# Optimization experiments

Measured on AMD Instinct MI355X. Metric: run time of the kernel, lower is better.

## Reference

```python
import jax, jax.numpy as jnp
import numpy as np

N_NODES = 100000
N_EDGES = 1600000
IN_F, HID_F, OUT_F = 128, 128, 64


def setup_inputs() -> dict:
    key = jax.random.key(0)
    ks = jax.random.split(key, 12)
    inp = {
        "features": jax.random.normal(ks[0], (N_NODES, IN_F), dtype=jnp.float32),
        "src": jax.random.randint(ks[1], (N_EDGES,), 0, N_NODES, dtype=jnp.int32),
        "dst": jax.random.randint(ks[2], (N_EDGES,), 0, N_NODES, dtype=jnp.int32),
        "Ws0": jax.random.normal(ks[3], (IN_F, HID_F), dtype=jnp.float32) / np.sqrt(IN_F),
        "Wn0": jax.random.normal(ks[4], (IN_F, HID_F), dtype=jnp.float32) / np.sqrt(IN_F),
        "b0": jnp.zeros((HID_F,), dtype=jnp.float32),
        "Ws1": jax.random.normal(ks[5], (HID_F, HID_F), dtype=jnp.float32) / np.sqrt(HID_F),
        "Wn1": jax.random.normal(ks[6], (HID_F, HID_F), dtype=jnp.float32) / np.sqrt(HID_F),
        "b1": jnp.zeros((HID_F,), dtype=jnp.float32),
        "Ws2": jax.random.normal(ks[7], (HID_F, OUT_F), dtype=jnp.float32) / np.sqrt(HID_F),
        "Wn2": jax.random.normal(ks[8], (HID_F, OUT_F), dtype=jnp.float32) / np.sqrt(HID_F),
        "b2": jnp.zeros((OUT_F,), dtype=jnp.float32),
    }
    return inp


def _sage_conv(h, src, dst, inv_deg, Ws, Wn, b, act):
    # gather neighbor (source) features along edges: [E, d]
    msg = h[src]
    # mean aggregation onto destination nodes: [N, d]
    agg = jax.ops.segment_sum(msg, dst, num_segments=N_NODES) * inv_deg
    out = h @ Ws + agg @ Wn + b
    return jax.nn.relu(out) if act else out


def reference(features, src, dst, Ws0, Wn0, b0, Ws1, Wn1, b1, Ws2, Wn2, b2):
    # in-degree for mean normalization (clamped at 1, matching DGL mean semantics)
    deg = jax.ops.segment_sum(jnp.ones((N_EDGES,), jnp.float32), dst, num_segments=N_NODES)
    inv_deg = (1.0 / jnp.maximum(deg, 1.0))[:, None]
    h = _sage_conv(features, src, dst, inv_deg, Ws0, Wn0, b0, act=True)
    # dropout is identity in eval mode
    h = _sage_conv(h, src, dst, inv_deg, Ws1, Wn1, b1, act=True)
    h = _sage_conv(h, src, dst, inv_deg, Ws2, Wn2, b2, act=False)
    return h
```

## Files before the change

### kernel.cpp

```cpp
#include <hip/hip_runtime.h>

static constexpr int N = 100000;
static constexpr int E = 1600000;
static constexpr int F = 128;
static constexpr int HA_W = 256;
static constexpr int NB = (N + 127) / 128;
static constexpr int PCHUNK = 16384;
static constexpr int PGRID = (E + PCHUNK - 1) / PCHUNK;
static constexpr int CAP = 8192;

typedef __attribute__((ext_vector_type(8))) short bf16x8;
typedef __attribute__((ext_vector_type(4))) float f32x4;

__device__ inline unsigned short f2bf(float f) {
    unsigned int u = __builtin_bit_cast(unsigned int, f);
    unsigned int r = u + 0x7FFF + ((u >> 16) & 1);
    return (unsigned short)(r >> 16);
}
__device__ inline float bf_lo(unsigned int v) {
    return __builtin_bit_cast(float, v << 16);
}
__device__ inline float bf_hi(unsigned int v) {
    return __builtin_bit_cast(float, v & 0xffff0000u);
}

__global__ __launch_bounds__(256) void bucket_count_k(const int* __restrict__ dst,
                                                      int* __restrict__ bcnt) {
    __shared__ int sh[NB];
    const int t = threadIdx.x;
    for (int i = t; i < NB; i += 256) sh[i] = 0;
    __syncthreads();
    const int cb = blockIdx.x * PCHUNK;
    #pragma unroll
    for (int j = 0; j < PCHUNK / 1024; ++j) {
        int idx = cb + j * 1024 + t * 4;
        if (idx < E) {
            int4 d4 = *(const int4*)&dst[idx];
            atomicAdd(&sh[d4.x >> 7], 1);
            atomicAdd(&sh[d4.y >> 7], 1);
            atomicAdd(&sh[d4.z >> 7], 1);
            atomicAdd(&sh[d4.w >> 7], 1);
        }
    }
    __syncthreads();
    for (int i = t; i < NB; i += 256)
        if (sh[i]) atomicAdd(&bcnt[i], sh[i]);
}

__global__ __launch_bounds__(1024) void scan_buckets_k(const int* __restrict__ bcnt,
                                                       int* __restrict__ bbase,
                                                       int* __restrict__ bcur,
                                                       int* __restrict__ row_ptr) {
    __shared__ int shw[16];
    const int t = threadIdx.x, lane = t & 63, wv = t >> 6;
    int v = (t < NB) ? bcnt[t] : 0;
    int s = v;
    #pragma unroll
    for (int off = 1; off < 64; off <<= 1) {
        int u = __shfl_up(s, off);
        if (lane >= off) s += u;
    }
    if (lane == 63) shw[wv] = s;
    __syncthreads();
    if (wv == 0 && lane < 16) {
        int w = shw[lane];
        #pragma unroll
        for (int off = 1; off < 16; off <<= 1) {
            int u = __shfl_up(w, off);
            if (lane >= off) w += u;
        }
        shw[lane] = w;
    }
    __syncthreads();
    int wex = wv ? shw[wv - 1] : 0;
    int excl = wex + s - v;
    if (t < NB) { bbase[t] = excl; bcur[t] = 0; }
    if (t == 0) { bbase[NB] = E; row_ptr[N] = E; }
}

__global__ __launch_bounds__(256) void partition_k(const int* __restrict__ src,
                                                   const int* __restrict__ dst,
                                                   const int* __restrict__ bbase,
                                                   int* __restrict__ bcur,
                                                   unsigned int* __restrict__ ebuf) {
    __shared__ int sh_hist[NB];
    __shared__ int sh_base[NB];
    __shared__ int sh_cur[NB];
    const int t = threadIdx.x;
    for (int i = t; i < NB; i += 256) sh_hist[i] = 0;
    __syncthreads();
    const int cb = blockIdx.x * PCHUNK;
    #pragma unroll
    for (int j = 0; j < PCHUNK / 1024; ++j) {
        int idx = cb + j * 1024 + t * 4;
        if (idx < E) {
            int4 d4 = *(const int4*)&dst[idx];
            atomicAdd(&sh_hist[d4.x >> 7], 1);
            atomicAdd(&sh_hist[d4.y >> 7], 1);
            atomicAdd(&sh_hist[d4.z >> 7], 1);
            atomicAdd(&sh_hist[d4.w >> 7], 1);
        }
    }
    __syncthreads();
    for (int i = t; i < NB; i += 256) {
        int c = sh_hist[i];
        sh_base[i] = c ? (bbase[i] + atomicAdd(&bcur[i], c)) : 0;
        sh_cur[i] = 0;
    }
    __syncthreads();
    #pragma unroll
    for (int j = 0; j < PCHUNK / 1024; ++j) {
        int idx = cb + j * 1024 + t * 4;
        if (idx < E) {
            int4 s4 = *(const int4*)&src[idx];
            int4 d4 = *(const int4*)&dst[idx];
            {
                int b = d4.x >> 7; int p = atomicAdd(&sh_cur[b], 1);
                ebuf[sh_base[b] + p] = (unsigned)s4.x | ((unsigned)(d4.x & 127) << 17);
            }
            {
                int b = d4.y >> 7; int p = atomicAdd(&sh_cur[b], 1);
                ebuf[sh_base[b] + p] = (unsigned)s4.y | ((unsigned)(d4.y & 127) << 17);
            }
            {
                int b = d4.z >> 7; int p = atomicAdd(&sh_cur[b], 1);
                ebuf[sh_base[b] + p] = (unsigned)s4.z | ((unsigned)(d4.z & 127) << 17);
            }
            {
                int b = d4.w >> 7; int p = atomicAdd(&sh_cur[b], 1);
                ebuf[sh_base[b] + p] = (unsigned)s4.w | ((unsigned)(d4.w & 127) << 17);
            }
        }
    }
}

__global__ __launch_bounds__(256) void csr_sort_k(const unsigned int* __restrict__ ebuf,
                                                  const int* __restrict__ bbase,
                                                  int* __restrict__ row_ptr,
                                                  float* __restrict__ inv_deg,
                                                  int* __restrict__ esrc) {
    __shared__ unsigned int sh_e[CAP];
    __shared__ int sh_o[CAP];
    __shared__ int sh_hist[128];
    __shared__ int sh_excl[128];
    __shared__ int sh_cur[128];
    __shared__ int sh_w0;
    const int b = blockIdx.x, t = threadIdx.x;
    const int e0 = bbase[b];
    const int ec = bbase[b + 1] - e0;
    if (t < 128) { sh_hist[t] = 0; sh_cur[t] = 0; }
    __syncthreads();
    for (int i = t; i < ec; i += 256) {
        unsigned int e = ebuf[e0 + i];
        sh_e[i] = e;
        atomicAdd(&sh_hist[e >> 17], 1);
    }
    __syncthreads();
    int v = 0;
    if (t < 128) v = sh_hist[t];
    int incl = v;
    const int lane = t & 63;
    #pragma unroll
    for (int off = 1; off < 64; off <<= 1) {
        int u = __shfl_up(incl, off);
        if (lane >= off) incl += u;
    }
    if (t == 63) sh_w0 = incl;
    __syncthreads();
    if (t >= 64 && t < 128) incl += sh_w0;
    if (t < 128) {
        sh_excl[t] = incl - v;
        int node = b * 128 + t;
        if (node < N) {
            row_ptr[node] = e0 + incl - v;
            inv_deg[node] = 1.0f / fmaxf((float)v, 1.0f);
        }
    }
    __syncthreads();
    for (int i = t; i < ec; i += 256) {
        unsigned int e = sh_e[i];
        int l = e >> 17;
        int pos = sh_excl[l] + atomicAdd(&sh_cur[l], 1);
        sh_o[pos] = (int)(e & 0x1FFFF);
    }
    __syncthreads();
    for (int i = t; i < ec; i += 256) esrc[e0 + i] = sh_o[i];
}

__global__ __launch_bounds__(256) void conv_feat_k(const float* __restrict__ feat,
                                                   unsigned short* __restrict__ ha) {
    int idx = blockIdx.x * 256 + threadIdx.x;
    int node = idx >> 5;
    int c4 = idx & 31;
    if (node >= N) return;
    float4 v = *(const float4*)&feat[(size_t)node * F + c4 * 4];
    unsigned long long p = (unsigned long long)f2bf(v.x)
                         | ((unsigned long long)f2bf(v.y) << 16)
                         | ((unsigned long long)f2bf(v.z) << 32)
                         | ((unsigned long long)f2bf(v.w) << 48);
    *(unsigned long long*)&ha[(size_t)node * HA_W + c4 * 4] = p;
}

__global__ __launch_bounds__(256) void prep_w_all_k(const float* __restrict__ Ws0,
                                                    const float* __restrict__ Wn0,
                                                    const float* __restrict__ Ws1,
                                                    const float* __restrict__ Wn1,
                                                    const float* __restrict__ Ws2,
                                                    const float* __restrict__ Wn2,
                                                    unsigned short* __restrict__ Wt0,
                                                    unsigned short* __restrict__ Wt1,
                                                    unsigned short* __restrict__ Wc2) {
    int idx = blockIdx.x * 256 + threadIdx.x;
    if (idx < 32768) {
        int n = idx >> 8, k = idx & 255;
        float v = (k < 128) ? Ws0[k * 128 + n] : Wn0[(k - 128) * 128 + n];
        Wt0[n * 256 + k] = f2bf(v);
    } else if (idx < 65536) {
        int j = idx - 32768;
        int n = j >> 8, k = j & 255;
        float v = (k < 128) ? Ws1[k * 128 + n] : Wn1[(k - 128) * 128 + n];
        Wt1[n * 256 + k] = f2bf(v);
    } else if (idx < 65536 + 16384) {
        int j = idx - 65536;
        int c = j >> 7, k = j & 127;
        float v = (c < 64) ? Ws2[k * 64 + c] : Wn2[k * 64 + (c - 64)];
        Wc2[c * 128 + k] = f2bf(v);
    }
}

__global__ __launch_bounds__(256) void aggregate128_k(const unsigned short* __restrict__ ha,
                                                      unsigned short* __restrict__ ha_out,
                                                      const int* __restrict__ row_ptr,
                                                      const int* __restrict__ esrc,
                                                      const float* __restrict__ inv_deg) {
    const int lane = threadIdx.x & 63;
    const int wv = threadIdx.x >> 6;
    const int slot = lane >> 4;
    const int cl = lane & 15;
    const int node = blockIdx.x * 16 + wv * 4 + slot;
    const int beg = row_ptr[node];
    const int cnt = row_ptr[node + 1] - beg;
    const float sinv = inv_deg[node];
    int wmax = cnt;
    wmax = max(wmax, __shfl_xor(wmax, 16));
    wmax = max(wmax, __shfl_xor(wmax, 32));
    float a0 = 0.f, a1 = 0.f, a2 = 0.f, a3 = 0.f;
    float a4 = 0.f, a5 = 0.f, a6 = 0.f, a7 = 0.f;
    for (int j = 0; j < wmax; j += 8) {
        int idx[8];
        uint4 v[8];
        #pragma unroll
        for (int u = 0; u < 8; ++u)
            idx[u] = (j + u < cnt) ? __builtin_nontemporal_load(&esrc[beg + j + u]) : -1;
        #pragma unroll
        for (int u = 0; u < 8; ++u) {
            if (idx[u] >= 0)
                v[u] = *(const uint4*)&ha[(size_t)idx[u] * HA_W + cl * 8];
            else { v[u].x = 0u; v[u].y = 0u; v[u].z = 0u; v[u].w = 0u; }
        }
        #pragma unroll
        for (int u = 0; u < 8; ++u) {
            a0 += bf_lo(v[u].x); a1 += bf_hi(v[u].x);
            a2 += bf_lo(v[u].y); a3 += bf_hi(v[u].y);
            a4 += bf_lo(v[u].z); a5 += bf_hi(v[u].z);
            a6 += bf_lo(v[u].w); a7 += bf_hi(v[u].w);
        }
    }
    uint4 o;
    o.x = (unsigned int)f2bf(a0 * sinv) | ((unsigned int)f2bf(a1 * sinv) << 16);
    o.y = (unsigned int)f2bf(a2 * sinv) | ((unsigned int)f2bf(a3 * sinv) << 16);
    o.z = (unsigned int)f2bf(a4 * sinv) | ((unsigned int)f2bf(a5 * sinv) << 16);
    o.w = (unsigned int)f2bf(a6 * sinv) | ((unsigned int)f2bf(a7 * sinv) << 16);
    *(uint4*)&ha_out[(size_t)node * HA_W + F + cl * 8] = o;
}

__global__ __launch_bounds__(256) void aggregate64_add_k(const unsigned short* __restrict__ Q,
                                                         const int* __restrict__ row_ptr,
                                                         const int* __restrict__ esrc,
                                                         const float* __restrict__ inv_deg,
                                                         float* __restrict__ out) {
    const int lane = threadIdx.x & 63;
    const int wv = threadIdx.x >> 6;
    const int slot = lane >> 3;
    const int cl = lane & 7;
    const int node = blockIdx.x * 32 + wv * 8 + slot;
    const int beg = row_ptr[node];
    const int cnt = row_ptr[node + 1] - beg;
    const float sinv = inv_deg[node];
    int wmax = cnt;
    wmax = max(wmax, __shfl_xor(wmax, 8));
    wmax = max(wmax, __shfl_xor(wmax, 16));
    wmax = max(wmax, __shfl_xor(wmax, 32));
    float a0 = 0.f, a1 = 0.f, a2 = 0.f, a3 = 0.f;
    float a4 = 0.f, a5 = 0.f, a6 = 0.f, a7 = 0.f;
    for (int j = 0; j < wmax; j += 8) {
        int idx[8];
        uint4 v[8];
        #pragma unroll
        for (int u = 0; u < 8; ++u)
            idx[u] = (j + u < cnt) ? __builtin_nontemporal_load(&esrc[beg + j + u]) : -1;
        #pragma unroll
        for (int u = 0; u < 8; ++u) {
            if (idx[u] >= 0)
                v[u] = *(const uint4*)&Q[(size_t)idx[u] * 64 + cl * 8];
            else { v[u].x = 0u; v[u].y = 0u; v[u].z = 0u; v[u].w = 0u; }
        }
        #pragma unroll
        for (int u = 0; u < 8; ++u) {
            a0 += bf_lo(v[u].x); a1 += bf_hi(v[u].x);
            a2 += bf_lo(v[u].y); a3 += bf_hi(v[u].y);
            a4 += bf_lo(v[u].z); a5 += bf_hi(v[u].z);
            a6 += bf_lo(v[u].w); a7 += bf_hi(v[u].w);
        }
    }
    float4* p0 = (float4*)&out[(size_t)node * 64 + cl * 8];
    float4 pv = *p0;
    pv.x += a0 * sinv; pv.y += a1 * sinv; pv.z += a2 * sinv; pv.w += a3 * sinv;
    *p0 = pv;
    float4* p1 = p0 + 1;
    float4 pw = *p1;
    pw.x += a4 * sinv; pw.y += a5 * sinv; pw.z += a6 * sinv; pw.w += a7 * sinv;
    *p1 = pw;
}

__global__ __launch_bounds__(256) void linear01_k(const unsigned short* __restrict__ ha,
                                                  const unsigned short* __restrict__ Wt,
                                                  const float* __restrict__ bias,
                                                  unsigned short* __restrict__ out_ha) {
    constexpr int CPW = 32;
    constexpr int NT = 2;
    const int lane = threadIdx.x & 63;
    const int wv = threadIdx.x >> 6;
    const int col0 = wv * CPW;
    const int lc = lane & 15;
    const int lg = lane >> 4;
    bf16x8 bfrag[NT][8];
    float bias_c[NT];
    #pragma unroll
    for (int nt = 0; nt < NT; ++nt) {
        int col = col0 + nt * 16 + lc;
        bias_c[nt] = bias[col];
        #pragma unroll
        for (int ks = 0; ks < 8; ++ks)
            bfrag[nt][ks] = *(const bf16x8*)&Wt[col * 256 + ks * 32 + lg * 8];
    }
    const int i0base = blockIdx.x * 128;
    for (int s = 0; s < 8; ++s) {
        int i0 = i0base + s * 16;
        if (i0 >= N) return;
        const unsigned short* arow = &ha[(size_t)(i0 + lc) * HA_W];
        f32x4 acc[NT];
        #pragma unroll
        for (int nt = 0; nt < NT; ++nt) {
            acc[nt][0] = bias_c[nt]; acc[nt][1] = bias_c[nt];
            acc[nt][2] = bias_c[nt]; acc[nt][3] = bias_c[nt];
        }
        #pragma unroll
        for (int ks = 0; ks < 8; ++ks) {
            bf16x8 af = *(const bf16x8*)&arow[ks * 32 + lg * 8];
            #pragma unroll
            for (int nt = 0; nt < NT; ++nt)
                acc[nt] = __builtin_amdgcn_mfma_f32_16x16x32_bf16(af, bfrag[nt][ks], acc[nt], 0, 0, 0);
        }
        #pragma unroll
        for (int nt = 0; nt < NT; ++nt) {
            int col = col0 + nt * 16 + lc;
            #pragma unroll
            for (int r = 0; r < 4; ++r) {
                int orow = i0 + lg * 4 + r;
                float v = fmaxf(acc[nt][r], 0.f);
                out_ha[(size_t)orow * HA_W + col] = f2bf(v);
            }
        }
    }
}

__global__ __launch_bounds__(256) void linear2_k(const unsigned short* __restrict__ ha,
                                                 const unsigned short* __restrict__ Wc,
                                                 const float* __restrict__ bias,
                                                 float* __restrict__ out,
                                                 unsigned short* __restrict__ Q) {
    constexpr int CPW = 32;
    constexpr int NT = 2;
    const int lane = threadIdx.x & 63;
    const int wv = threadIdx.x >> 6;
    const int col0 = wv * CPW;
    const int lc = lane & 15;
    const int lg = lane >> 4;
    bf16x8 bfrag[NT][4];
    float bias_c[NT];
    #pragma unroll
    for (int nt = 0; nt < NT; ++nt) {
        int col = col0 + nt * 16 + lc;
        bias_c[nt] = (wv < 2) ? bias[col] : 0.f;
        #pragma unroll
        for (int ks = 0; ks < 4; ++ks)
            bfrag[nt][ks] = *(const bf16x8*)&Wc[col * 128 + ks * 32 + lg * 8];
    }
    const int i0base = blockIdx.x * 128;
    for (int s = 0; s < 8; ++s) {
        int i0 = i0base + s * 16;
        if (i0 >= N) return;
        const unsigned short* arow = &ha[(size_t)(i0 + lc) * HA_W];
        f32x4 acc[NT];
        #pragma unroll
        for (int nt = 0; nt < NT; ++nt) {
            acc[nt][0] = bias_c[nt]; acc[nt][1] = bias_c[nt];
            acc[nt][2] = bias_c[nt]; acc[nt][3] = bias_c[nt];
        }
        #pragma unroll
        for (int ks = 0; ks < 4; ++ks) {
            bf16x8 af = *(const bf16x8*)&arow[ks * 32 + lg * 8];
            #pragma unroll
            for (int nt = 0; nt < NT; ++nt)
                acc[nt] = __builtin_amdgcn_mfma_f32_16x16x32_bf16(af, bfrag[nt][ks], acc[nt], 0, 0, 0);
        }
        #pragma unroll
        for (int nt = 0; nt < NT; ++nt) {
            int col = col0 + nt * 16 + lc;
            #pragma unroll
            for (int r = 0; r < 4; ++r) {
                int orow = i0 + lg * 4 + r;
                float v = acc[nt][r];
                if (wv < 2) out[(size_t)orow * 64 + col] = v;
                else        Q[(size_t)orow * 64 + (col - 64)] = f2bf(v);
            }
        }
    }
}

extern "C" void kernel_launch(void* const* d_in, const int* in_sizes, int n_in,
                              void* d_out, int out_size, void* d_ws, size_t ws_size,
                              hipStream_t stream) {
    const float* feat = (const float*)d_in[0];
    const int*   src  = (const int*)d_in[1];
    const int*   dst  = (const int*)d_in[2];
    const float* Ws0  = (const float*)d_in[3];
    const float* Wn0  = (const float*)d_in[4];
    const float* b0   = (const float*)d_in[5];
    const float* Ws1  = (const float*)d_in[6];
    const float* Wn1  = (const float*)d_in[7];
    const float* b1   = (const float*)d_in[8];
    const float* Ws2  = (const float*)d_in[9];
    const float* Wn2  = (const float*)d_in[10];
    const float* b2   = (const float*)d_in[11];
    float* out = (float*)d_out;

    char* ws = (char*)d_ws;
    size_t off = 0;
    auto alloc = [&](size_t bytes) {
        void* p = ws + off;
        off = (off + bytes + 255) & ~(size_t)255;
        return p;
    };
    unsigned short* haA = (unsigned short*)alloc((size_t)N * HA_W * 2);
    unsigned short* haB = (unsigned short*)alloc((size_t)N * HA_W * 2);
    unsigned short* Qb  = (unsigned short*)alloc((size_t)N * 64 * 2);
    unsigned short* Wt0 = (unsigned short*)alloc((size_t)128 * 256 * 2);
    unsigned short* Wt1 = (unsigned short*)alloc((size_t)128 * 256 * 2);
    unsigned short* Wc2 = (unsigned short*)alloc((size_t)128 * 128 * 2);
    float* inv     = (float*)alloc((size_t)N * 4);
    int*   row_ptr = (int*)alloc((size_t)(N + 1) * 4);
    int*   bcnt    = (int*)alloc((size_t)NB * 4);
    int*   bbase   = (int*)alloc((size_t)(NB + 1) * 4);
    int*   bcur    = (int*)alloc((size_t)NB * 4);
    unsigned int* ebuf = (unsigned int*)alloc((size_t)E * 4);
    int*   esrc    = (int*)alloc((size_t)E * 4);
    (void)ws_size; (void)in_sizes; (void)n_in; (void)out_size;

    hipMemsetAsync(bcnt, 0, (size_t)NB * 4, stream);
    bucket_count_k<<<PGRID, 256, 0, stream>>>(dst, bcnt);
    scan_buckets_k<<<1, 1024, 0, stream>>>(bcnt, bbase, bcur, row_ptr);
    partition_k<<<PGRID, 256, 0, stream>>>(src, dst, bbase, bcur, ebuf);
    csr_sort_k<<<NB, 256, 0, stream>>>(ebuf, bbase, row_ptr, inv, esrc);

    conv_feat_k<<<(N * 32 + 255) / 256, 256, 0, stream>>>(feat, haA);
    prep_w_all_k<<<(65536 + 16384 + 255) / 256, 256, 0, stream>>>(
        Ws0, Wn0, Ws1, Wn1, Ws2, Wn2, Wt0, Wt1, Wc2);

    const int lin_grid = (N + 127) / 128;
    aggregate128_k<<<N / 16, 256, 0, stream>>>(haA, haA, row_ptr, esrc, inv);
    linear01_k<<<lin_grid, 256, 0, stream>>>(haA, Wt0, b0, haB);
    aggregate128_k<<<N / 16, 256, 0, stream>>>(haB, haB, row_ptr, esrc, inv);
    linear01_k<<<lin_grid, 256, 0, stream>>>(haB, Wt1, b1, haA);
    linear2_k<<<lin_grid, 256, 0, stream>>>(haA, Wc2, b2, out, Qb);
    aggregate64_add_k<<<N / 32, 256, 0, stream>>>(Qb, row_ptr, esrc, inv, out);
}
```

Before: 326.1 us.

## Fuse aggregation with linear layer via LDS and merge prep kernels

Fuses mean-aggregation and the dense linear for layers 0 and 1 into one 512-thread kernel. Each block aggregates 128 nodes into shared memory and then runs MFMA on the self features from global memory plus the aggregated tile from LDS. The feature buffers shrink from 256 to 128 columns because the aggregate no longer round-trips through global memory. Feature conversion, bucket counting and weight prep are merged into one launch. The fused kernel has only NB (~782) blocks, which may cut gather parallelism and latency hiding compared with the old 6250-block aggregate kernel.

New measurement: 328.5 us. About the same (+0.8%).

```diff
diff --git a/kernel.cpp b/kernel.cpp
--- a/kernel.cpp
+++ b/kernel.cpp
@@ -3,11 +3,11 @@
 static constexpr int N = 100000;
 static constexpr int E = 1600000;
 static constexpr int F = 128;
-static constexpr int HA_W = 256;
 static constexpr int NB = (N + 127) / 128;
 static constexpr int PCHUNK = 16384;
 static constexpr int PGRID = (E + PCHUNK - 1) / PCHUNK;
 static constexpr int CAP = 8192;
+static constexpr int NPAD = NB * 128;
 
 typedef __attribute__((ext_vector_type(8))) short bf16x8;
 typedef __attribute__((ext_vector_type(4))) float f32x4;
@@ -24,27 +24,70 @@
     return __builtin_bit_cast(float, v & 0xffff0000u);
 }
 
-__global__ __launch_bounds__(256) void bucket_count_k(const int* __restrict__ dst,
-                                                      int* __restrict__ bcnt) {
+__global__ __launch_bounds__(256) void prep_all_k(const float* __restrict__ feat,
+                                                  unsigned short* __restrict__ hA,
+                                                  const int* __restrict__ dst,
+                                                  int* __restrict__ bcnt,
+                                                  const float* __restrict__ Ws0,
+                                                  const float* __restrict__ Wn0,
+                                                  const float* __restrict__ Ws1,
+                                                  const float* __restrict__ Wn1,
+                                                  const float* __restrict__ Ws2,
+                                                  const float* __restrict__ Wn2,
+                                                  unsigned short* __restrict__ Wt0,
+                                                  unsigned short* __restrict__ Wt1,
+                                                  unsigned short* __restrict__ Wc2) {
     __shared__ int sh[NB];
     const int t = threadIdx.x;
-    for (int i = t; i < NB; i += 256) sh[i] = 0;
-    __syncthreads();
-    const int cb = blockIdx.x * PCHUNK;
-    #pragma unroll
-    for (int j = 0; j < PCHUNK / 1024; ++j) {
-        int idx = cb + j * 1024 + t * 4;
-        if (idx < E) {
-            int4 d4 = *(const int4*)&dst[idx];
-            atomicAdd(&sh[d4.x >> 7], 1);
-            atomicAdd(&sh[d4.y >> 7], 1);
-            atomicAdd(&sh[d4.z >> 7], 1);
-            atomicAdd(&sh[d4.w >> 7], 1);
-        }
-    }
-    __syncthreads();
-    for (int i = t; i < NB; i += 256)
-        if (sh[i]) atomicAdd(&bcnt[i], sh[i]);
+    const int bid = blockIdx.x;
+    if (bid < 12500) {
+        int idx = bid * 256 + t;
+        int node = idx >> 5;
+        int c4 = idx & 31;
+        if (node < N) {
+            float4 v = *(const float4*)&feat[(size_t)node * F + c4 * 4];
+            unsigned long long p = (unsigned long long)f2bf(v.x)
+                                 | ((unsigned long long)f2bf(v.y) << 16)
+                                 | ((unsigned long long)f2bf(v.z) << 32)
+                                 | ((unsigned long long)f2bf(v.w) << 48);
+            *(unsigned long long*)&hA[(size_t)node * F + c4 * 4] = p;
+        }
+    } else if (bid < 12500 + PGRID) {
+        for (int i = t; i < NB; i += 256) sh[i] = 0;
+        __syncthreads();
+        const int cb = (bid - 12500) * PCHUNK;
+        #pragma unroll
+        for (int j = 0; j < PCHUNK / 1024; ++j) {
+            int idx = cb + j * 1024 + t * 4;
+            if (idx < E) {
+                int4 d4 = *(const int4*)&dst[idx];
+                atomicAdd(&sh[d4.x >> 7], 1);
+                atomicAdd(&sh[d4.y >> 7], 1);
+                atomicAdd(&sh[d4.z >> 7], 1);
+                atomicAdd(&sh[d4.w >> 7], 1);
+            }
+        }
+        __syncthreads();
+        for (int i = t; i < NB; i += 256)
+            if (sh[i]) atomicAdd(&bcnt[i], sh[i]);
+    } else {
+        int idx = (bid - 12500 - PGRID) * 256 + t;
+        if (idx < 32768) {
+            int n = idx >> 8, k = idx & 255;
+            float v = (k < 128) ? Ws0[k * 128 + n] : Wn0[(k - 128) * 128 + n];
+            Wt0[n * 256 + k] = f2bf(v);
+        } else if (idx < 65536) {
+            int j = idx - 32768;
+            int n = j >> 8, k = j & 255;
+            float v = (k < 128) ? Ws1[k * 128 + n] : Wn1[(k - 128) * 128 + n];
+            Wt1[n * 256 + k] = f2bf(v);
+        } else if (idx < 65536 + 16384) {
+            int j = idx - 65536;
+            int c = j >> 7, k = j & 127;
+            float v = (c < 64) ? Ws2[k * 64 + c] : Wn2[k * 64 + (c - 64)];
+            Wc2[c * 128 + k] = f2bf(v);
+        }
+    }
 }
 
 __global__ __launch_bounds__(1024) void scan_buckets_k(const int* __restrict__ bcnt,
@@ -187,91 +230,146 @@
     for (int i = t; i < ec; i += 256) esrc[e0 + i] = sh_o[i];
 }
 
-__global__ __launch_bounds__(256) void conv_feat_k(const float* __restrict__ feat,
-                                                   unsigned short* __restrict__ ha) {
-    int idx = blockIdx.x * 256 + threadIdx.x;
-    int node = idx >> 5;
-    int c4 = idx & 31;
-    if (node >= N) return;
-    float4 v = *(const float4*)&feat[(size_t)node * F + c4 * 4];
-    unsigned long long p = (unsigned long long)f2bf(v.x)
-                         | ((unsigned long long)f2bf(v.y) << 16)
-                         | ((unsigned long long)f2bf(v.z) << 32)
-                         | ((unsigned long long)f2bf(v.w) << 48);
-    *(unsigned long long*)&ha[(size_t)node * HA_W + c4 * 4] = p;
-}
-
-__global__ __launch_bounds__(256) void prep_w_all_k(const float* __restrict__ Ws0,
-                                                    const float* __restrict__ Wn0,
-                                                    const float* __restrict__ Ws1,
-                                                    const float* __restrict__ Wn1,
-                                                    const float* __restrict__ Ws2,
-                                                    const float* __restrict__ Wn2,
-                                                    unsigned short* __restrict__ Wt0,
-                                                    unsigned short* __restrict__ Wt1,
-                                                    unsigned short* __restrict__ Wc2) {
-    int idx = blockIdx.x * 256 + threadIdx.x;
-    if (idx < 32768) {
-        int n = idx >> 8, k = idx & 255;
-        float v = (k < 128) ? Ws0[k * 128 + n] : Wn0[(k - 128) * 128 + n];
-        Wt0[n * 256 + k] = f2bf(v);
-    } else if (idx < 65536) {
-        int j = idx - 32768;
-        int n = j >> 8, k = j & 255;
-        float v = (k < 128) ? Ws1[k * 128 + n] : Wn1[(k - 128) * 128 + n];
-        Wt1[n * 256 + k] = f2bf(v);
-    } else if (idx < 65536 + 16384) {
-        int j = idx - 65536;
-        int c = j >> 7, k = j & 127;
-        float v = (c < 64) ? Ws2[k * 64 + c] : Wn2[k * 64 + (c - 64)];
-        Wc2[c * 128 + k] = f2bf(v);
-    }
-}
-
-__global__ __launch_bounds__(256) void aggregate128_k(const unsigned short* __restrict__ ha,
-                                                      unsigned short* __restrict__ ha_out,
-                                                      const int* __restrict__ row_ptr,
-                                                      const int* __restrict__ esrc,
-                                                      const float* __restrict__ inv_deg) {
+__global__ __launch_bounds__(512) void fused_layer_k(const unsigned short* __restrict__ h,
+                                                     const unsigned short* __restrict__ Wt,
+                                                     const float* __restrict__ bias,
+                                                     unsigned short* __restrict__ hout,
+                                                     const int* __restrict__ row_ptr,
+                                                     const int* __restrict__ esrc,
+                                                     const float* __restrict__ inv_deg) {
+    __shared__ unsigned short agg[128][136];
     const int lane = threadIdx.x & 63;
     const int wv = threadIdx.x >> 6;
     const int slot = lane >> 4;
     const int cl = lane & 15;
-    const int node = blockIdx.x * 16 + wv * 4 + slot;
-    const int beg = row_ptr[node];
-    const int cnt = row_ptr[node + 1] - beg;
-    const float sinv = inv_deg[node];
-    int wmax = cnt;
-    wmax = max(wmax, __shfl_xor(wmax, 16));
-    wmax = max(wmax, __shfl_xor(wmax, 32));
-    float a0 = 0.f, a1 = 0.f, a2 = 0.f, a3 = 0.f;
-    float a4 = 0.f, a5 = 0.f, a6 = 0.f, a7 = 0.f;
-    for (int j = 0; j < wmax; j += 8) {
-        int idx[8];
-        uint4 v[8];
-        #pragma unroll
-        for (int u = 0; u < 8; ++u)
-            idx[u] = (j + u < cnt) ? __builtin_nontemporal_load(&esrc[beg + j + u]) : -1;
-        #pragma unroll
-        for (int u = 0; u < 8; ++u) {
-            if (idx[u] >= 0)
-                v[u] = *(const uint4*)&ha[(size_t)idx[u] * HA_W + cl * 8];
-            else { v[u].x = 0u; v[u].y = 0u; v[u].z = 0u; v[u].w = 0u; }
-        }
-        #pragma unroll
-        for (int u = 0; u < 8; ++u) {
-            a0 += bf_lo(v[u].x); a1 += bf_hi(v[u].x);
-            a2 += bf_lo(v[u].y); a3 += bf_hi(v[u].y);
-            a4 += bf_lo(v[u].z); a5 += bf_hi(v[u].z);
-            a6 += bf_lo(v[u].w); a7 += bf_hi(v[u].w);
-        }
-    }
-    uint4 o;
-    o.x = (unsigned int)f2bf(a0 * sinv) | ((unsigned int)f2bf(a1 * sinv) << 16);
-    o.y = (unsigned int)f2bf(a2 * sinv) | ((unsigned int)f2bf(a3 * sinv) << 16);
-    o.z = (unsigned int)f2bf(a4 * sinv) | ((unsigned int)f2bf(a5 * sinv) << 16);
-    o.w = (unsigned int)f2bf(a6 * sinv) | ((unsigned int)f2bf(a7 * sinv) << 16);
-    *(uint4*)&ha_out[(size_t)node * HA_W + F + cl * 8] = o;
+    const int nbase = blockIdx.x * 128;
+    #pragma unroll
+    for (int pass = 0; pass < 4; ++pass) {
+        const int nloc = wv * 16 + pass * 4 + slot;
+        const int node = nbase + nloc;
+        int beg = 0, cnt = 0;
+        float sinv = 0.f;
+        if (node < N) {
+            beg = row_ptr[node];
+            cnt = row_ptr[node + 1] - beg;
+            sinv = inv_deg[node];
+        }
+        int wmax = cnt;
+        wmax = max(wmax, __shfl_xor(wmax, 16));
+        wmax = max(wmax, __shfl_xor(wmax, 32));
+        float a0 = 0.f, a1 = 0.f, a2 = 0.f, a3 = 0.f;
+        float a4 = 0.f, a5 = 0.f, a6 = 0.f, a7 = 0.f;
+        for (int j = 0; j < wmax; j += 8) {
+            int idx[8];
+            uint4 v[8];
+            #pragma unroll
+            for (int u = 0; u < 8; ++u)
+                idx[u] = (j + u < cnt) ? __builtin_nontemporal_load(&esrc[beg + j + u]) : -1;
+            #pragma unroll
+            for (int u = 0; u < 8; ++u) {
+                if (idx[u] >= 0)
+                    v[u] = *(const uint4*)&h[(size_t)idx[u] * F + cl * 8];
+                else { v[u].x = 0u; v[u].y = 0u; v[u].z = 0u; v[u].w = 0u; }
+            }
+            #pragma unroll
+            for (int u = 0; u < 8; ++u) {
+                a0 += bf_lo(v[u].x); a1 += bf_hi(v[u].x);
+                a2 += bf_lo(v[u].y); a3 += bf_hi(v[u].y);
+                a4 += bf_lo(v[u].z); a5 += bf_hi(v[u].z);
+                a6 += bf_lo(v[u].w); a7 += bf_hi(v[u].w);
+            }
+        }
+        uint4 o;
+        o.x = (unsigned int)f2bf(a0 * sinv) | ((unsigned int)f2bf(a1 * sinv) << 16);
+        o.y = (unsigned int)f2bf(a2 * sinv) | ((unsigned int)f2bf(a3 * sinv) << 16);
+        o.z = (unsigned int)f2bf(a4 * sinv) | ((unsigned int)f2bf(a5 * sinv) << 16);
+        o.w = (unsigned int)f2bf(a6 * sinv) | ((unsigned int)f2bf(a7 * sinv) << 16);
+        *(uint4*)&agg[nloc][cl * 8] = o;
+    }
+    __syncthreads();
+    const int lc = lane & 15;
+    const int lg = lane >> 4;
+    const int col = wv * 16 + lc;
+    bf16x8 bfrag[8];
+    #pragma unroll
+    for (int ks = 0; ks < 8; ++ks)
+        bfrag[ks] = *(const bf16x8*)&Wt[col * 256 + ks * 32 + lg * 8];
+    const float bias_c = bias[col];
+    for (int s = 0; s < 8; ++s) {
+        int i0 = nbase + s * 16;
+        if (i0 >= N) break;
+        f32x4 acc;
+        acc[0] = bias_c; acc[1] = bias_c; acc[2] = bias_c; acc[3] = bias_c;
+        #pragma unroll
+        for (int ks = 0; ks < 4; ++ks) {
+            bf16x8 af = *(const bf16x8*)&h[(size_t)(i0 + lc) * F + ks * 32 + lg * 8];
+            acc = __builtin_amdgcn_mfma_f32_16x16x32_bf16(af, bfrag[ks], acc, 0, 0, 0);
+        }
+        #pragma unroll
+        for (int ks = 0; ks < 4; ++ks) {
+            bf16x8 af = *(const bf16x8*)&agg[s * 16 + lc][ks * 32 + lg * 8];
+            acc = __builtin_amdgcn_mfma_f32_16x16x32_bf16(af, bfrag[ks + 4], acc, 0, 0, 0);
+        }
+        #pragma unroll
+        for (int r = 0; r < 4; ++r) {
+            int orow = i0 + lg * 4 + r;
+            hout[(size_t)orow * F + col] = f2bf(fmaxf(acc[r], 0.f));
+        }
+    }
+}
+
+__global__ __launch_bounds__(256) void linear2_k(const unsigned short* __restrict__ h,
+                                                 const unsigned short* __restrict__ Wc,
+                                                 const float* __restrict__ bias,
+                                                 float* __restrict__ out,
+                                                 unsigned short* __restrict__ Q) {
+    constexpr int CPW = 32;
+    constexpr int NT = 2;
+    const int lane = threadIdx.x & 63;
+    const int wv = threadIdx.x >> 6;
+    const int col0 = wv * CPW;
+    const int lc = lane & 15;
+    const int lg = lane >> 4;
+    bf16x8 bfrag[NT][4];
+    float bias_c[NT];
+    #pragma unroll
+    for (int nt = 0; nt < NT; ++nt) {
+        int col = col0 + nt * 16 + lc;
+        bias_c[nt] = (wv < 2) ? bias[col] : 0.f;
+        #pragma unroll
+        for (int ks = 0; ks < 4; ++ks)
+            bfrag[nt][ks] = *(const bf16x8*)&Wc[col * 128 + ks * 32 + lg * 8];
+    }
+    const int i0base = blockIdx.x * 128;
+    for (int s = 0; s < 8; ++s) {
+        int i0 = i0base + s * 16;
+        if (i0 >= N) return;
+        const unsigned short* arow = &h[(size_t)(i0 + lc) * F];
+        f32x4 acc[NT];
+        #pragma unroll
+        for (int nt = 0; nt < NT; ++nt) {
+            acc[nt][0] = bias_c[nt]; acc[nt][1] = bias_c[nt];
+            acc[nt][2] = bias_c[nt]; acc[nt][3] = bias_c[nt];
+        }
+        #pragma unroll
+        for (int ks = 0; ks < 4; ++ks) {
+            bf16x8 af = *(const bf16x8*)&arow[ks * 32 + lg * 8];
+            #pragma unroll
+            for (int nt = 0; nt < NT; ++nt)
+                acc[nt] = __builtin_amdgcn_mfma_f32_16x16x32_bf16(af, bfrag[nt][ks], acc[nt], 0, 0, 0);
+        }
+        #pragma unroll
+        for (int nt = 0; nt < NT; ++nt) {
+            int col = col0 + nt * 16 + lc;
+            #pragma unroll
+            for (int r = 0; r < 4; ++r) {
+                int orow = i0 + lg * 4 + r;
+                float v = acc[nt][r];
+                if (wv < 2) out[(size_t)orow * 64 + col] = v;
+                else        Q[(size_t)orow * 64 + (col - 64)] = f2bf(v);
+            }
+        }
+    }
 }
 
 __global__ __launch_bounds__(256) void aggregate64_add_k(const unsigned short* __restrict__ Q,
@@ -323,112 +421,6 @@
     *p1 = pw;
 }
 
-__global__ __launch_bounds__(256) void linear01_k(const unsigned short* __restrict__ ha,
-                                                  const unsigned short* __restrict__ Wt,
-                                                  const float* __restrict__ bias,
-                                                  unsigned short* __restrict__ out_ha) {
-    constexpr int CPW = 32;
-    constexpr int NT = 2;
-    const int lane = threadIdx.x & 63;
-    const int wv = threadIdx.x >> 6;
-    const int col0 = wv * CPW;
-    const int lc = lane & 15;
-    const int lg = lane >> 4;
-    bf16x8 bfrag[NT][8];
-    float bias_c[NT];
-    #pragma unroll
-    for (int nt = 0; nt < NT; ++nt) {
-        int col = col0 + nt * 16 + lc;
-        bias_c[nt] = bias[col];
-        #pragma unroll
-        for (int ks = 0; ks < 8; ++ks)
-            bfrag[nt][ks] = *(const bf16x8*)&Wt[col * 256 + ks * 32 + lg * 8];
-    }
-    const int i0base = blockIdx.x * 128;
-    for (int s = 0; s < 8; ++s) {
-        int i0 = i0base + s * 16;
-        if (i0 >= N) return;
-        const unsigned short* arow = &ha[(size_t)(i0 + lc) * HA_W];
-        f32x4 acc[NT];
-        #pragma unroll
-        for (int nt = 0; nt < NT; ++nt) {
-            acc[nt][0] = bias_c[nt]; acc[nt][1] = bias_c[nt];
-            acc[nt][2] = bias_c[nt]; acc[nt][3] = bias_c[nt];
-        }
-        #pragma unroll
-        for (int ks = 0; ks < 8; ++ks) {
-            bf16x8 af = *(const bf16x8*)&arow[ks * 32 + lg * 8];
-            #pragma unroll
-            for (int nt = 0; nt < NT; ++nt)
-                acc[nt] = __builtin_amdgcn_mfma_f32_16x16x32_bf16(af, bfrag[nt][ks], acc[nt], 0, 0, 0);
-        }
-        #pragma unroll
-        for (int nt = 0; nt < NT; ++nt) {
-            int col = col0 + nt * 16 + lc;
-            #pragma unroll
-            for (int r = 0; r < 4; ++r) {
-                int orow = i0 + lg * 4 + r;
-                float v = fmaxf(acc[nt][r], 0.f);
-                out_ha[(size_t)orow * HA_W + col] = f2bf(v);
-            }
-        }
-    }
-}
-
-__global__ __launch_bounds__(256) void linear2_k(const unsigned short* __restrict__ ha,
-                                                 const unsigned short* __restrict__ Wc,
-                                                 const float* __restrict__ bias,
-                                                 float* __restrict__ out,
-                                                 unsigned short* __restrict__ Q) {
-    constexpr int CPW = 32;
-    constexpr int NT = 2;
-    const int lane = threadIdx.x & 63;
-    const int wv = threadIdx.x >> 6;
-    const int col0 = wv * CPW;
-    const int lc = lane & 15;
-    const int lg = lane >> 4;
-    bf16x8 bfrag[NT][4];
-    float bias_c[NT];
-    #pragma unroll
-    for (int nt = 0; nt < NT; ++nt) {
-        int col = col0 + nt * 16 + lc;
-        bias_c[nt] = (wv < 2) ? bias[col] : 0.f;
-        #pragma unroll
-        for (int ks = 0; ks < 4; ++ks)
-            bfrag[nt][ks] = *(const bf16x8*)&Wc[col * 128 + ks * 32 + lg * 8];
-    }
-    const int i0base = blockIdx.x * 128;
-    for (int s = 0; s < 8; ++s) {
-        int i0 = i0base + s * 16;
-        if (i0 >= N) return;
-        const unsigned short* arow = &ha[(size_t)(i0 + lc) * HA_W];
-        f32x4 acc[NT];
-        #pragma unroll
-        for (int nt = 0; nt < NT; ++nt) {
-            acc[nt][0] = bias_c[nt]; acc[nt][1] = bias_c[nt];
-            acc[nt][2] = bias_c[nt]; acc[nt][3] = bias_c[nt];
-        }
-        #pragma unroll
-        for (int ks = 0; ks < 4; ++ks) {
-            bf16x8 af = *(const bf16x8*)&arow[ks * 32 + lg * 8];
-            #pragma unroll
-            for (int nt = 0; nt < NT; ++nt)
-                acc[nt] = __builtin_amdgcn_mfma_f32_16x16x32_bf16(af, bfrag[nt][ks], acc[nt], 0, 0, 0);
-        }
-        #pragma unroll
-        for (int nt = 0; nt < NT; ++nt) {
-            int col = col0 + nt * 16 + lc;
-            #pragma unroll
-            for (int r = 0; r < 4; ++r) {
-                int orow = i0 + lg * 4 + r;
-                float v = acc[nt][r];
-                if (wv < 2) out[(size_t)orow * 64 + col] = v;
-                else        Q[(size_t)orow * 64 + (col - 64)] = f2bf(v);
-            }
-        }
-    }
-}
-
 extern "C" void kernel_launch(void* const* d_in, const int* in_sizes, int n_in,
                               void* d_out, int out_size, void* d_ws, size_t ws_size,
                               hipStream_t stream) {
@@ -453,8 +445,8 @@
         off = (off + bytes + 255) & ~(size_t)255;
         return p;
     };
-    unsigned short* haA = (unsigned short*)alloc((size_t)N * HA_W * 2);
-    unsigned short* haB = (unsigned short*)alloc((size_t)N * HA_W * 2);
+    unsigned short* hA  = (unsigned short*)alloc((size_t)NPAD * F * 2);
+    unsigned short* hB  = (unsigned short*)alloc((size_t)NPAD * F * 2);
     unsigned short* Qb  = (unsigned short*)alloc((size_t)N * 64 * 2);
     unsigned short* Wt0 = (unsigned short*)alloc((size_t)128 * 256 * 2);
     unsigned short* Wt1 = (unsigned short*)alloc((size_t)128 * 256 * 2);
@@ -469,20 +461,16 @@
     (void)ws_size; (void)in_sizes; (void)n_in; (void)out_size;
 
     hipMemsetAsync(bcnt, 0, (size_t)NB * 4, stream);
-    bucket_count_k<<<PGRID, 256, 0, stream>>>(dst, bcnt);
+    prep_all_k<<<12500 + PGRID + 320, 256, 0, stream>>>(
+        feat, hA, dst, bcnt, Ws0, Wn0, Ws1, Wn1, Ws2, Wn2, Wt0, Wt1, Wc2);
+
     scan_buckets_k<<<1, 1024, 0, stream>>>(bcnt, bbase, bcur, row_ptr);
     partition_k<<<PGRID, 256, 0, stream>>>(src, dst, bbase, bcur, ebuf);
     csr_sort_k<<<NB, 256, 0, stream>>>(ebuf, bbase, row_ptr, inv, esrc);
 
-    conv_feat_k<<<(N * 32 + 255) / 256, 256, 0, stream>>>(feat, haA);
-    prep_w_all_k<<<(65536 + 16384 + 255) / 256, 256, 0, stream>>>(
-        Ws0, Wn0, Ws1, Wn1, Ws2, Wn2, Wt0, Wt1, Wc2);
-
-    const int lin_grid = (N + 127) / 128;
-    aggregate128_k<<<N / 16, 256, 0, stream>>>(haA, haA, row_ptr, esrc, inv);
-    linear01_k<<<lin_grid, 256, 0, stream>>>(haA, Wt0, b0, haB);
-    aggregate128_k<<<N / 16, 256, 0, stream>>>(haB, haB, row_ptr, esrc, inv);
-    linear01_k<<<lin_grid, 256, 0, stream>>>(haB, Wt1, b1, haA);
-    linear2_k<<<lin_grid, 256, 0, stream>>>(haA, Wc2, b2, out, Qb);
+    fused_layer_k<<<NB, 512, 0, stream>>>(hA, Wt0, b0, hB, row_ptr, esrc, inv);
+    fused_layer_k<<<NB, 512, 0, stream>>>(hB, Wt1, b1, hA, row_ptr, esrc, inv);
+
+    linear2_k<<<NB, 256, 0, stream>>>(hA, Wc2, b2, out, Qb);
     aggregate64_add_k<<<N / 32, 256, 0, stream>>>(Qb, row_ptr, esrc, inv, out);
 }
```
